# Kernel tuning notes

Hardware: AMD Instinct MI355X
Metric: run time of the kernel (lower is better)

Reference implementation:

```python
import jax, jax.numpy as jnp
import numpy as np

WH, WW = 7, 7
N = WH * WW
DIM = 256
HEADS = 8
HEAD_DIM = DIM // HEADS
SCALE = HEAD_DIM ** -0.5


def _relative_position_index():
    coords = np.stack(np.meshgrid(np.arange(WH), np.arange(WW), indexing='ij'))  # [2,Wh,Ww]
    cf = coords.reshape(2, -1)                      # [2,N]
    rel = cf[:, :, None] - cf[:, None, :]           # [2,N,N]
    rel = rel.transpose(1, 2, 0)                    # [N,N,2]
    rel[..., 0] += WH - 1
    rel[..., 1] += WW - 1
    rel[..., 0] *= 2 * WW - 1
    return rel.sum(-1)                              # [N,N] in [0, (2Wh-1)(2Ww-1))

_REL_IDX = jnp.asarray(_relative_position_index())


def setup_inputs() -> dict:
    key = jax.random.key(0)
    ks = jax.random.split(key, 6)
    B_ = 8192
    return {
        'x': jax.random.normal(ks[0], (B_, N, DIM), dtype=jnp.float32),
        'qkv_w': jax.random.normal(ks[1], (3 * DIM, DIM), dtype=jnp.float32) * 0.02,
        'qkv_b': jax.random.normal(ks[2], (3 * DIM,), dtype=jnp.float32) * 0.02,
        'proj_w': jax.random.normal(ks[3], (DIM, DIM), dtype=jnp.float32) * 0.02,
        'proj_b': jax.random.normal(ks[4], (DIM,), dtype=jnp.float32) * 0.02,
        'bias_table': jax.random.normal(ks[5], ((2 * WH - 1) * (2 * WW - 1), HEADS), dtype=jnp.float32) * 0.02,
    }


def reference(x, qkv_w, qkv_b, proj_w, proj_b, bias_table):
    B_, n, C = x.shape
    # QKV projection -> [3, B_, H, N, hd]
    qkv = (x @ qkv_w.T + qkv_b).reshape(B_, n, 3, HEADS, HEAD_DIM)
    qkv = jnp.transpose(qkv, (2, 0, 3, 1, 4))
    q, k, v = qkv[0], qkv[1], qkv[2]
    # Gathered relative position bias: [H, N, N]
    bias = bias_table[_REL_IDX.reshape(-1)].reshape(n, n, HEADS).transpose(2, 0, 1)
    # Scaled dot-product attention with additive bias
    attn = jnp.einsum('bhnd,bhmd->bhnm', q, k) * SCALE + bias[None]
    attn = jax.nn.softmax(attn, axis=-1)
    out = jnp.einsum('bhnm,bhmd->bhnd', attn, v)
    out = jnp.transpose(out, (0, 2, 1, 3)).reshape(B_, n, C)
    return out @ proj_w.T + proj_b
```

## Files before the change

### kernel.cpp

```cpp
#include <hip/hip_runtime.h>
#include <hip/hip_bf16.h>
#include <stdint.h>

#define NTOK 49
#define SCALE 0.17677669529663687f

typedef __attribute__((ext_vector_type(8))) short bf16x8;
typedef __attribute__((ext_vector_type(4))) float f32x4;

__device__ __forceinline__ unsigned short f2bf(float f) {
    union { float f; unsigned int u; } v; v.f = f;
    unsigned int r = v.u + 0x7FFFu + ((v.u >> 16) & 1u);
    return (unsigned short)(r >> 16);
}

__device__ __forceinline__ uint32_t pkbf(float lo, float hi) {
    __hip_bfloat162 h = __float22bfloat162_rn(float2{lo, hi});
    union { __hip_bfloat162 h; uint32_t u; } c; c.h = h;
    return c.u;
}

__global__ void prep_kernel(const float* __restrict__ qkv_w,
                            const float* __restrict__ proj_w,
                            const float* __restrict__ bias_table,
                            const float* __restrict__ qkv_b,
                            unsigned short* __restrict__ w_qkv,
                            unsigned short* __restrict__ w_proj,
                            float* __restrict__ bias_t,
                            float* __restrict__ sbias) {
    const int total = 196608 + 65536 + 32768 + 768;
    for (int i = blockIdx.x * blockDim.x + threadIdx.x; i < total;
         i += gridDim.x * blockDim.x) {
        if (i < 196608) {
            float s = (i < 65536) ? SCALE : 1.0f;
            w_qkv[i] = f2bf(qkv_w[i] * s);
        } else if (i < 262144) {
            w_proj[i - 196608] = f2bf(proj_w[i - 196608]);
        } else if (i < 294912) {
            int idx = i - 262144;
            int hh = idx >> 12;
            int j  = (idx >> 6) & 63;
            int ii = idx & 63;
            float v;
            if (j >= NTOK)       v = -1e30f;
            else if (ii >= NTOK) v = 0.0f;
            else {
                int rel = (ii / 7 - j / 7 + 6) * 13 + (ii % 7 - j % 7 + 6);
                v = bias_table[rel * 8 + hh];
            }
            bias_t[idx] = v;
        } else {
            int r = i - 294912;
            sbias[r] = qkv_b[r] * (r < 256 ? SCALE : 1.0f);
        }
    }
}

__global__ __launch_bounds__(512, 4) void wattn_kernel(
    const float* __restrict__ x,
    const unsigned short* __restrict__ w_qkv,
    const unsigned short* __restrict__ w_proj,
    const float* __restrict__ bias_t,
    const float* __restrict__ sbias,
    const float* __restrict__ proj_b,
    float* __restrict__ out)
{
    extern __shared__ char smem[];
    unsigned short* sX = (unsigned short*)smem;
    unsigned short* scrBase = sX + 64 * 264;

    const int tid  = threadIdx.x;
    const int wv   = tid >> 6;
    const int lane = tid & 63;
    const int l16  = lane & 15;
    const int g    = lane >> 4;
    const int lk   = g * 8;

    unsigned short* scr = scrBase + wv * (32 * 72);
    unsigned short* sO  = sX;
    const int b = blockIdx.x;
    const int h = wv;
    const f32x4 fz = {0.f, 0.f, 0.f, 0.f};

    const float* xb = x + (size_t)b * (NTOK * 256);
    for (int it = tid * 4; it < NTOK * 256; it += 512 * 4) {
        float4 v = *(const float4*)(xb + it);
        int r = it >> 8, c = it & 255;
        uint2 u = make_uint2(pkbf(v.x, v.y), pkbf(v.z, v.w));
        *(uint2*)(sX + r * 264 + c) = u;
    }
    for (int it = tid * 4; it < 15 * 256; it += 512 * 4) {
        int r = 49 + (it >> 8), c = it & 255;
        *(uint2*)(sX + r * 264 + c) = make_uint2(0, 0);
    }
    __syncthreads();

    bf16x8 qf[4], kf[4], vf[2][2];

    {
        f32x4 acc[4][4];
        #pragma unroll
        for (int mt = 0; mt < 4; ++mt)
            #pragma unroll
            for (int nt = 0; nt < 4; ++nt) acc[mt][nt] = fz;

        for (int kb = 0; kb < 8; ++kb) {
            bf16x8 bx[4];
            #pragma unroll
            for (int nt = 0; nt < 4; ++nt)
                bx[nt] = *(const bf16x8*)(sX + (nt * 16 + l16) * 264 + kb * 32 + lk);
            #pragma unroll
            for (int mt = 0; mt < 4; ++mt) {
                const int row = (mt < 2) ? (h * 32 + mt * 16 + l16)
                                         : (256 + h * 32 + (mt - 2) * 16 + l16);
                bf16x8 aw = *(const bf16x8*)(w_qkv + row * 256 + kb * 32 + lk);
                #pragma unroll
                for (int nt = 0; nt < 4; ++nt)
                    acc[mt][nt] = __builtin_amdgcn_mfma_f32_16x16x32_bf16(
                        aw, bx[nt], acc[mt][nt], 0, 0, 0);
            }
        }
        float4 bq0 = *(const float4*)(sbias + h * 32 + 4 * g);
        float4 bq1 = *(const float4*)(sbias + h * 32 + 16 + 4 * g);
        #pragma unroll
        for (int nt = 0; nt < 4; ++nt) {
            acc[0][nt][0] += bq0.x; acc[0][nt][1] += bq0.y;
            acc[0][nt][2] += bq0.z; acc[0][nt][3] += bq0.w;
            acc[1][nt][0] += bq1.x; acc[1][nt][1] += bq1.y;
            acc[1][nt][2] += bq1.z; acc[1][nt][3] += bq1.w;
        }
        #pragma unroll
        for (int bt = 0; bt < 2; ++bt) {
            #pragma unroll
            for (int mt = 0; mt < 4; ++mt) {
                #pragma unroll
                for (int ntl = 0; ntl < 2; ++ntl) {
                    const int nt = bt * 2 + ntl;
                    uint2 d = make_uint2(pkbf(acc[mt][nt][0], acc[mt][nt][1]),
                                         pkbf(acc[mt][nt][2], acc[mt][nt][3]));
                    *(uint2*)(scr + (ntl * 16 + l16) * 72 + mt * 16 + 4 * g) = d;
                }
            }
            #pragma unroll
            for (int ntl = 0; ntl < 2; ++ntl) {
                qf[bt * 2 + ntl] = *(const bf16x8*)(scr + (ntl * 16 + l16) * 72 + lk);
                kf[bt * 2 + ntl] = *(const bf16x8*)(scr + (ntl * 16 + l16) * 72 + 32 + lk);
            }
        }
    }

    {
        f32x4 acc[4][2];
        #pragma unroll
        for (int rt = 0; rt < 4; ++rt) { acc[rt][0] = fz; acc[rt][1] = fz; }

        for (int kb = 0; kb < 8; ++kb) {
            bf16x8 ax[4];
            #pragma unroll
            for (int rt = 0; rt < 4; ++rt)
                ax[rt] = *(const bf16x8*)(sX + (rt * 16 + l16) * 264 + kb * 32 + lk);
            #pragma unroll
            for (int ct = 0; ct < 2; ++ct) {
                bf16x8 bw = *(const bf16x8*)(w_qkv + (512 + h * 32 + ct * 16 + l16) * 256 + kb * 32 + lk);
                #pragma unroll
                for (int rt = 0; rt < 4; ++rt)
                    acc[rt][ct] = __builtin_amdgcn_mfma_f32_16x16x32_bf16(
                        ax[rt], bw, acc[rt][ct], 0, 0, 0);
            }
        }
        #pragma unroll
        for (int rt = 0; rt < 4; ++rt)
            #pragma unroll
            for (int ct = 0; ct < 2; ++ct) {
                uint2 d = make_uint2(pkbf(acc[rt][ct][0], acc[rt][ct][1]),
                                     pkbf(acc[rt][ct][2], acc[rt][ct][3]));
                *(uint2*)(scr + (ct * 16 + l16) * 72 + rt * 16 + 4 * g) = d;
            }
        #pragma unroll
        for (int dm = 0; dm < 2; ++dm)
            #pragma unroll
            for (int kk = 0; kk < 2; ++kk)
                vf[dm][kk] = *(const bf16x8*)(scr + (dm * 16 + l16) * 72 + kk * 32 + lk);
    }
    __syncthreads();

    const float* bt_h = bias_t + h * 4096;
    float4 bv0 = *(const float4*)(sbias + 512 + h * 32 + 4 * g);
    float4 bv1 = *(const float4*)(sbias + 512 + h * 32 + 16 + 4 * g);

    #pragma unroll
    for (int hf = 0; hf < 2; ++hf) {
        f32x4 s[4][2];
        #pragma unroll
        for (int tr = 0; tr < 4; ++tr)
            #pragma unroll
            for (int tl = 0; tl < 2; ++tl) {
                const int i = (hf * 2 + tl) * 16 + l16;
                #pragma unroll
                for (int r = 0; r < 4; ++r)
                    s[tr][tl][r] = bt_h[(tr * 16 + 4 * g + r) * 64 + i];
            }
        #pragma unroll
        for (int tr = 0; tr < 4; ++tr)
            #pragma unroll
            for (int tl = 0; tl < 2; ++tl)
                s[tr][tl] = __builtin_amdgcn_mfma_f32_16x16x32_bf16(
                    kf[tr], qf[hf * 2 + tl], s[tr][tl], 0, 0, 0);

        float inv[2];
        #pragma unroll
        for (int tl = 0; tl < 2; ++tl) {
            float mx = s[0][tl][0];
            #pragma unroll
            for (int tr = 0; tr < 4; ++tr)
                #pragma unroll
                for (int r = 0; r < 4; ++r) mx = fmaxf(mx, s[tr][tl][r]);
            mx = fmaxf(mx, __shfl_xor(mx, 16));
            mx = fmaxf(mx, __shfl_xor(mx, 32));
            float sum = 0.f;
            #pragma unroll
            for (int tr = 0; tr < 4; ++tr)
                #pragma unroll
                for (int r = 0; r < 4; ++r) {
                    float e = __expf(s[tr][tl][r] - mx);
                    s[tr][tl][r] = e; sum += e;
                }
            sum += __shfl_xor(sum, 16);
            sum += __shfl_xor(sum, 32);
            inv[tl] = 1.0f / sum;
        }

        #pragma unroll
        for (int tr = 0; tr < 4; ++tr)
            #pragma unroll
            for (int tl = 0; tl < 2; ++tl) {
                uint2 d = make_uint2(pkbf(s[tr][tl][0], s[tr][tl][1]),
                                     pkbf(s[tr][tl][2], s[tr][tl][3]));
                *(uint2*)(scr + (tl * 16 + l16) * 72 + tr * 16 + 4 * g) = d;
            }
        bf16x8 pf[2][2];
        #pragma unroll
        for (int tl = 0; tl < 2; ++tl)
            #pragma unroll
            for (int kk = 0; kk < 2; ++kk)
                pf[tl][kk] = *(const bf16x8*)(scr + (tl * 16 + l16) * 72 + kk * 32 + lk);

        f32x4 o[2][2];
        #pragma unroll
        for (int dm = 0; dm < 2; ++dm) { o[dm][0] = fz; o[dm][1] = fz; }
        #pragma unroll
        for (int dm = 0; dm < 2; ++dm)
            #pragma unroll
            for (int tl = 0; tl < 2; ++tl)
                #pragma unroll
                for (int kk = 0; kk < 2; ++kk)
                    o[dm][tl] = __builtin_amdgcn_mfma_f32_16x16x32_bf16(
                        vf[dm][kk], pf[tl][kk], o[dm][tl], 0, 0, 0);

        #pragma unroll
        for (int dm = 0; dm < 2; ++dm) {
            const float4 bv = dm ? bv1 : bv0;
            #pragma unroll
            for (int tl = 0; tl < 2; ++tl) {
                const float iv = inv[tl];
                float r0 = o[dm][tl][0] * iv + bv.x;
                float r1 = o[dm][tl][1] * iv + bv.y;
                float r2 = o[dm][tl][2] * iv + bv.z;
                float r3 = o[dm][tl][3] * iv + bv.w;
                uint2 d = make_uint2(pkbf(r0, r1), pkbf(r2, r3));
                *(uint2*)(sO + ((hf * 2 + tl) * 16 + l16) * 264 + h * 32 + dm * 16 + 4 * g) = d;
            }
        }
    }
    __syncthreads();

    {
        f32x4 acc[4][2];
        #pragma unroll
        for (int rt = 0; rt < 4; ++rt) { acc[rt][0] = fz; acc[rt][1] = fz; }

        const int colbase = wv * 32;
        for (int kb = 0; kb < 8; ++kb) {
            bf16x8 a[4];
            #pragma unroll
            for (int rt = 0; rt < 4; ++rt)
                a[rt] = *(const bf16x8*)(sO + (rt * 16 + l16) * 264 + kb * 32 + lk);
            #pragma unroll
            for (int c = 0; c < 2; ++c) {
                bf16x8 bw = *(const bf16x8*)(w_proj + (colbase + c * 16 + l16) * 256 + kb * 32 + lk);
                #pragma unroll
                for (int rt = 0; rt < 4; ++rt)
                    acc[rt][c] = __builtin_amdgcn_mfma_f32_16x16x32_bf16(
                        a[rt], bw, acc[rt][c], 0, 0, 0);
            }
        }
        float* ob = out + (size_t)b * (NTOK * 256);
        #pragma unroll
        for (int c = 0; c < 2; ++c) {
            const int col = colbase + c * 16 + l16;
            const float pb = proj_b[col];
            #pragma unroll
            for (int rt = 0; rt < 4; ++rt)
                #pragma unroll
                for (int r = 0; r < 4; ++r) {
                    const int row = rt * 16 + 4 * g + r;
                    if (row < NTOK) ob[row * 256 + col] = acc[rt][c][r] + pb;
                }
        }
    }
}

extern "C" void kernel_launch(void* const* d_in, const int* in_sizes, int n_in,
                              void* d_out, int out_size, void* d_ws, size_t ws_size,
                              hipStream_t stream) {
    const float* x          = (const float*)d_in[0];
    const float* qkv_w      = (const float*)d_in[1];
    const float* qkv_b      = (const float*)d_in[2];
    const float* proj_w     = (const float*)d_in[3];
    const float* proj_b     = (const float*)d_in[4];
    const float* bias_table = (const float*)d_in[5];

    unsigned short* w_qkv  = (unsigned short*)d_ws;
    unsigned short* w_proj = w_qkv + 196608;
    float*          bias_t = (float*)(w_proj + 65536);
    float*          sbias  = bias_t + 32768;

    prep_kernel<<<288, 256, 0, stream>>>(qkv_w, proj_w, bias_table, qkv_b,
                                         w_qkv, w_proj, bias_t, sbias);

    const int SMEM = (64 * 264 + 8 * 32 * 72) * 2;
    hipFuncSetAttribute(reinterpret_cast<const void*>(wattn_kernel),
                        hipFuncAttributeMaxDynamicSharedMemorySize, SMEM);

    wattn_kernel<<<8192, 512, SMEM, stream>>>(x, w_qkv, w_proj, bias_t, sbias,
                                              proj_b, (float*)d_out);
}
```

Measured before the change: 720.8 us.

## Split Q and K projections into separate passes and repack scratch layout

Computes the Q and K projections in two separate GEMM loops with 2x4 accumulator tiles instead of one combined 4x4 loop, halving live accumulator registers. The per-wave scratch layout changes from 32x72 to 64x36 so each projection can be staged at once, and the softmax max/sum reductions become tree-shaped. The aim is lower register pressure and possibly higher occupancy, at the cost of reading the X tile from shared memory twice.

```diff
diff --git a/kernel.cpp b/kernel.cpp
--- a/kernel.cpp
+++ b/kernel.cpp
@@ -76,7 +76,7 @@
     const int g    = lane >> 4;
     const int lk   = g * 8;
 
-    unsigned short* scr = scrBase + wv * (32 * 72);
+    unsigned short* scr = scrBase + wv * (64 * 36);
     unsigned short* sO  = sX;
     const int b = blockIdx.x;
     const int h = wv;
@@ -98,9 +98,9 @@
     bf16x8 qf[4], kf[4], vf[2][2];
 
     {
-        f32x4 acc[4][4];
-        #pragma unroll
-        for (int mt = 0; mt < 4; ++mt)
+        f32x4 acc[2][4];
+        #pragma unroll
+        for (int mt = 0; mt < 2; ++mt)
             #pragma unroll
             for (int nt = 0; nt < 4; ++nt) acc[mt][nt] = fz;
 
@@ -110,10 +110,8 @@
             for (int nt = 0; nt < 4; ++nt)
                 bx[nt] = *(const bf16x8*)(sX + (nt * 16 + l16) * 264 + kb * 32 + lk);
             #pragma unroll
-            for (int mt = 0; mt < 4; ++mt) {
-                const int row = (mt < 2) ? (h * 32 + mt * 16 + l16)
-                                         : (256 + h * 32 + (mt - 2) * 16 + l16);
-                bf16x8 aw = *(const bf16x8*)(w_qkv + row * 256 + kb * 32 + lk);
+            for (int mt = 0; mt < 2; ++mt) {
+                bf16x8 aw = *(const bf16x8*)(w_qkv + (h * 32 + mt * 16 + l16) * 256 + kb * 32 + lk);
                 #pragma unroll
                 for (int nt = 0; nt < 4; ++nt)
                     acc[mt][nt] = __builtin_amdgcn_mfma_f32_16x16x32_bf16(
@@ -130,23 +128,50 @@
             acc[1][nt][2] += bq1.z; acc[1][nt][3] += bq1.w;
         }
         #pragma unroll
-        for (int bt = 0; bt < 2; ++bt) {
-            #pragma unroll
-            for (int mt = 0; mt < 4; ++mt) {
-                #pragma unroll
-                for (int ntl = 0; ntl < 2; ++ntl) {
-                    const int nt = bt * 2 + ntl;
-                    uint2 d = make_uint2(pkbf(acc[mt][nt][0], acc[mt][nt][1]),
-                                         pkbf(acc[mt][nt][2], acc[mt][nt][3]));
-                    *(uint2*)(scr + (ntl * 16 + l16) * 72 + mt * 16 + 4 * g) = d;
-                }
-            }
-            #pragma unroll
-            for (int ntl = 0; ntl < 2; ++ntl) {
-                qf[bt * 2 + ntl] = *(const bf16x8*)(scr + (ntl * 16 + l16) * 72 + lk);
-                kf[bt * 2 + ntl] = *(const bf16x8*)(scr + (ntl * 16 + l16) * 72 + 32 + lk);
-            }
-        }
+        for (int nt = 0; nt < 4; ++nt)
+            #pragma unroll
+            for (int mt = 0; mt < 2; ++mt) {
+                uint2 d = make_uint2(pkbf(acc[mt][nt][0], acc[mt][nt][1]),
+                                     pkbf(acc[mt][nt][2], acc[mt][nt][3]));
+                *(uint2*)(scr + (nt * 16 + l16) * 36 + mt * 16 + 4 * g) = d;
+            }
+        #pragma unroll
+        for (int nt = 0; nt < 4; ++nt)
+            qf[nt] = *(const bf16x8*)(scr + (nt * 16 + l16) * 36 + lk);
+    }
+
+    {
+        f32x4 acc[2][4];
+        #pragma unroll
+        for (int mt = 0; mt < 2; ++mt)
+            #pragma unroll
+            for (int nt = 0; nt < 4; ++nt) acc[mt][nt] = fz;
+
+        for (int kb = 0; kb < 8; ++kb) {
+            bf16x8 bx[4];
+            #pragma unroll
+            for (int nt = 0; nt < 4; ++nt)
+                bx[nt] = *(const bf16x8*)(sX + (nt * 16 + l16) * 264 + kb * 32 + lk);
+            #pragma unroll
+            for (int mt = 0; mt < 2; ++mt) {
+                bf16x8 aw = *(const bf16x8*)(w_qkv + (256 + h * 32 + mt * 16 + l16) * 256 + kb * 32 + lk);
+                #pragma unroll
+                for (int nt = 0; nt < 4; ++nt)
+                    acc[mt][nt] = __builtin_amdgcn_mfma_f32_16x16x32_bf16(
+                        aw, bx[nt], acc[mt][nt], 0, 0, 0);
+            }
+        }
+        #pragma unroll
+        for (int nt = 0; nt < 4; ++nt)
+            #pragma unroll
+            for (int mt = 0; mt < 2; ++mt) {
+                uint2 d = make_uint2(pkbf(acc[mt][nt][0], acc[mt][nt][1]),
+                                     pkbf(acc[mt][nt][2], acc[mt][nt][3]));
+                *(uint2*)(scr + (nt * 16 + l16) * 36 + mt * 16 + 4 * g) = d;
+            }
+        #pragma unroll
+        for (int nt = 0; nt < 4; ++nt)
+            kf[nt] = *(const bf16x8*)(scr + (nt * 16 + l16) * 36 + lk);
     }
 
     {
@@ -174,13 +199,13 @@
             for (int ct = 0; ct < 2; ++ct) {
                 uint2 d = make_uint2(pkbf(acc[rt][ct][0], acc[rt][ct][1]),
                                      pkbf(acc[rt][ct][2], acc[rt][ct][3]));
-                *(uint2*)(scr + (ct * 16 + l16) * 72 + rt * 16 + 4 * g) = d;
+                *(uint2*)(scr + ((rt >> 1) * 32 + ct * 16 + l16) * 36 + (rt & 1) * 16 + 4 * g) = d;
             }
         #pragma unroll
         for (int dm = 0; dm < 2; ++dm)
             #pragma unroll
             for (int kk = 0; kk < 2; ++kk)
-                vf[dm][kk] = *(const bf16x8*)(scr + (dm * 16 + l16) * 72 + kk * 32 + lk);
+                vf[dm][kk] = *(const bf16x8*)(scr + (kk * 32 + dm * 16 + l16) * 36 + lk);
     }
     __syncthreads();
 
@@ -210,21 +235,26 @@
         float inv[2];
         #pragma unroll
         for (int tl = 0; tl < 2; ++tl) {
-            float mx = s[0][tl][0];
+            float m4[4];
             #pragma unroll
             for (int tr = 0; tr < 4; ++tr)
-                #pragma unroll
-                for (int r = 0; r < 4; ++r) mx = fmaxf(mx, s[tr][tl][r]);
+                m4[tr] = fmaxf(fmaxf(s[tr][tl][0], s[tr][tl][1]),
+                               fmaxf(s[tr][tl][2], s[tr][tl][3]));
+            float mx = fmaxf(fmaxf(m4[0], m4[1]), fmaxf(m4[2], m4[3]));
             mx = fmaxf(mx, __shfl_xor(mx, 16));
             mx = fmaxf(mx, __shfl_xor(mx, 32));
-            float sum = 0.f;
-            #pragma unroll
-            for (int tr = 0; tr < 4; ++tr)
-                #pragma unroll
-                for (int r = 0; r < 4; ++r) {
-                    float e = __expf(s[tr][tl][r] - mx);
-                    s[tr][tl][r] = e; sum += e;
-                }
+            float s4[4];
+            #pragma unroll
+            for (int tr = 0; tr < 4; ++tr) {
+                float e0 = __expf(s[tr][tl][0] - mx);
+                float e1 = __expf(s[tr][tl][1] - mx);
+                float e2 = __expf(s[tr][tl][2] - mx);
+                float e3 = __expf(s[tr][tl][3] - mx);
+                s[tr][tl][0] = e0; s[tr][tl][1] = e1;
+                s[tr][tl][2] = e2; s[tr][tl][3] = e3;
+                s4[tr] = (e0 + e1) + (e2 + e3);
+            }
+            float sum = (s4[0] + s4[1]) + (s4[2] + s4[3]);
             sum += __shfl_xor(sum, 16);
             sum += __shfl_xor(sum, 32);
             inv[tl] = 1.0f / sum;
@@ -236,14 +266,14 @@
             for (int tl = 0; tl < 2; ++tl) {
                 uint2 d = make_uint2(pkbf(s[tr][tl][0], s[tr][tl][1]),
                                      pkbf(s[tr][tl][2], s[tr][tl][3]));
-                *(uint2*)(scr + (tl * 16 + l16) * 72 + tr * 16 + 4 * g) = d;
+                *(uint2*)(scr + ((tr >> 1) * 32 + tl * 16 + l16) * 36 + (tr & 1) * 16 + 4 * g) = d;
             }
         bf16x8 pf[2][2];
         #pragma unroll
         for (int tl = 0; tl < 2; ++tl)
             #pragma unroll
             for (int kk = 0; kk < 2; ++kk)
-                pf[tl][kk] = *(const bf16x8*)(scr + (tl * 16 + l16) * 72 + kk * 32 + lk);
+                pf[tl][kk] = *(const bf16x8*)(scr + (kk * 32 + tl * 16 + l16) * 36 + lk);
 
         f32x4 o[2][2];
         #pragma unroll
@@ -328,7 +358,7 @@
     prep_kernel<<<288, 256, 0, stream>>>(qkv_w, proj_w, bias_table, qkv_b,
                                          w_qkv, w_proj, bias_t, sbias);
 
-    const int SMEM = (64 * 264 + 8 * 32 * 72) * 2;
+    const int SMEM = (64 * 264 + 8 * 64 * 36) * 2;
     hipFuncSetAttribute(reinterpret_cast<const void*>(wattn_kernel),
                         hipFuncAttributeMaxDynamicSharedMemorySize, SMEM);
 
```

Result: slower. 834.7 us (+15.8%).
